# Optimization experiments

Measured on AMD Instinct MI355X. Metric: run time of the kernel, lower is better.

## Reference

```python
import jax, jax.numpy as jnp
import numpy as np

B = 2097152  # batch
H = 9        # hidden width
N_MID = 19   # fc2..fc20


def setup_inputs() -> dict:
    key = jax.random.key(0)
    ks = jax.random.split(key, 8)
    x = jax.random.normal(ks[0], (B, 2), dtype=jnp.float32)
    # PyTorch Linear init: U(-1/sqrt(fan_in), 1/sqrt(fan_in))
    def lin(k, out_f, in_f):
        kw, kb = jax.random.split(k)
        bound = 1.0 / np.sqrt(in_f)
        W = jax.random.uniform(kw, (out_f, in_f), jnp.float32, -bound, bound)
        b = jax.random.uniform(kb, (out_f,), jnp.float32, -bound, bound)
        return W, b
    W1, b1 = lin(ks[1], H, 2)
    # stacked middle layers fc2..fc20: [19, 9, 9] / [19, 9]
    kmids = jax.random.split(ks[2], N_MID)
    Wmid = jnp.stack([lin(k, H, H)[0] for k in kmids])
    bmid = jnp.stack([lin(jax.random.fold_in(k, 1), H, H)[1] for k in kmids])
    W21, b21 = lin(ks[3], 2, H)
    return {"x": x, "W1": W1, "b1": b1, "Wmid": Wmid, "bmid": bmid,
            "W21": W21, "b21": b21}


def reference(x, W1, b1, Wmid, bmid, W21, b21):
    h = jax.nn.elu(x @ W1.T + b1)  # [B, 9]
    def layer(h, wb):
        W, b = wb
        return jax.nn.elu(h @ W.T + b), None
    h, _ = jax.lax.scan(layer, h, (Wmid, bmid))
    logits = h @ W21.T + b21  # [B, 2]
    return jax.nn.log_softmax(logits, axis=1)
```

## Files before the change

kernel.cpp:

```cpp
#include <hip/hip_runtime.h>


typedef _Float16 half8 __attribute__((ext_vector_type(8)));
typedef float float4v __attribute__((ext_vector_type(4)));
typedef unsigned int uint4v __attribute__((ext_vector_type(4)));

constexpr int H   = 9;
constexpr int NL  = 21;
constexpr int TPW = 8;
constexpr int BLK = 256;

__global__ void build_frags(const float* __restrict__ W1, const float* __restrict__ b1,
                            const float* __restrict__ Wmid, const float* __restrict__ bmid,
                            const float* __restrict__ W21, const float* __restrict__ b21,
                            _Float16* __restrict__ ws) {
    const float L   = 1.4426950408889634f;
    const float LN2 = 0.6931471805599453f;
    int l    = blockIdx.x;
    int lane = threadIdx.x;
    int row  = lane & 15;
    int g    = lane >> 4;
    bool orow = ((row & 3) != 3) && (row < 12);
    int  o    = row - (row >> 2);
    for (int j = 0; j < 8; ++j) {
        int k = g * 8 + j;
        float v = 0.0f;
        if (l == 0) {
            if (orow && k < 2)        v = L * W1[o * 2 + k];
            else if (orow && k == 24) v = L * b1[o];
        } else if (l <= 19) {
            const float* W = Wmid + (l - 1) * 81;
            const float* b = bmid + (l - 1) * 9;
            if (orow) {
                if (j < 3 && g < 3) {
                    int r_in = g * 4 + j;
                    int i = r_in - (r_in >> 2);
                    v = W[o * 9 + i];
                } else if (j >= 4 && j < 7 && g < 3) {
                    int r_in = g * 4 + (j - 4);
                    int i = r_in - (r_in >> 2);
                    v = L * W[o * 9 + i];
                } else if (k == 24) {
                    float s = 0.0f;
                    for (int i = 0; i < H; ++i) s += W[o * 9 + i];
                    v = L * (b[o] - s);
                }
            }
        } else {
            if (row < 2) {
                if (j < 3 && g < 3) {
                    int r_in = g * 4 + j;
                    int i = r_in - (r_in >> 2);
                    v = LN2 * W21[row * 9 + i];
                } else if (j >= 4 && j < 7 && g < 3) {
                    int r_in = g * 4 + (j - 4);
                    int i = r_in - (r_in >> 2);
                    v = W21[row * 9 + i];
                } else if (k == 24) {
                    float s = 0.0f;
                    for (int i = 0; i < H; ++i) s += W21[row * 9 + i];
                    v = b21[row] - s;
                }
            }
        }
        ws[l * 512 + lane * 8 + j] = (_Float16)v;
    }
}

__device__ __forceinline__ half8 act_to_b(float4v d, unsigned bias_or) {
    float r0 = fmaxf(d[0], 0.f), r1 = fmaxf(d[1], 0.f), r2 = fmaxf(d[2], 0.f);
    float t0 = fminf(d[0], 0.f), t1 = fminf(d[1], 0.f), t2 = fminf(d[2], 0.f);
    float e0 = __builtin_amdgcn_exp2f(t0);
    float e1 = __builtin_amdgcn_exp2f(t1);
    float e2 = __builtin_amdgcn_exp2f(t2);
    uint4v u;
    u[0] = __builtin_bit_cast(unsigned, __builtin_amdgcn_cvt_pkrtz(r0, r1)) | bias_or;
    u[1] = __builtin_bit_cast(unsigned, __builtin_amdgcn_cvt_pkrtz(r2, 0.f));
    u[2] = __builtin_bit_cast(unsigned, __builtin_amdgcn_cvt_pkrtz(e0, e1));
    u[3] = __builtin_bit_cast(unsigned, __builtin_amdgcn_cvt_pkrtz(e2, 1.f));
    return __builtin_bit_cast(half8, u);
}

__device__ __forceinline__ half8 x_to_b(float2 xv, unsigned g0_sel, unsigned bias_or) {
    unsigned ux = __builtin_bit_cast(unsigned, __builtin_amdgcn_cvt_pkrtz(xv.x, xv.y));
    uint4v u;
    u[0] = (ux & g0_sel) | bias_or;
    u[1] = 0u; u[2] = 0u; u[3] = 0u;
    return __builtin_bit_cast(half8, u);
}

__device__ __forceinline__ float bperm(int byte_idx, float v) {
    return __builtin_bit_cast(float,
        __builtin_amdgcn_ds_bpermute(byte_idx, __builtin_bit_cast(int, v)));
}

__global__ __launch_bounds__(BLK, 2) void mlp_mfma(const float* __restrict__ x,
                                                   const _Float16* __restrict__ ws,
                                                   float* __restrict__ out) {
    const int lane = threadIdx.x & 63;
    const int wave = (blockIdx.x * BLK + threadIdx.x) >> 6;
    const int grp  = lane >> 4;
    const int col  = lane & 15;

    half8 A[NL];
    const half8* wsv = (const half8*)ws;
    #pragma unroll
    for (int l = 0; l < NL; ++l) A[l] = wsv[l * 64 + lane];

    const unsigned bias_or = (grp == 3) ? 0x00003C00u : 0u;
    const unsigned g0_sel  = (grp == 0) ? 0xFFFFFFFFu : 0u;
    const float4v ZV = {0.f, 0.f, 0.f, 0.f};
    const float NLOG2E = -1.4426950408889634f;
    const float LN2f   = 0.6931471805599453f;

    #pragma unroll 1
    for (int t = 0; t < TPW; t += 4) {
        const int tile0 = wave * TPW + t;

        half8 bf[4];
        #pragma unroll
        for (int k = 0; k < 4; ++k) {
            float2 xv = ((const float2*)x)[((tile0 + k) << 4) + col];
            bf[k] = x_to_b(xv, g0_sel, bias_or);
        }

        float4v dd[4];
        #pragma unroll
        for (int l = 0; l < NL; ++l) {
            #pragma unroll
            for (int k = 0; k < 4; ++k)
                dd[k] = __builtin_amdgcn_mfma_f32_16x16x32_f16(A[l], bf[k], ZV, 0, 0, 0);
            if (l < NL - 1) {
                #pragma unroll
                for (int k = 0; k < 4; ++k)
                    bf[k] = act_to_b(dd[k], bias_or);
            }
        }

        const int bidx = col << 2;
        float a0 = bperm(bidx, dd[0][0]), a1 = bperm(bidx, dd[0][1]);
        float b0 = bperm(bidx, dd[1][0]), b1 = bperm(bidx, dd[1][1]);
        float c0 = bperm(bidx, dd[2][0]), c1 = bperm(bidx, dd[2][1]);
        float d0 = bperm(bidx, dd[3][0]), d1 = bperm(bidx, dd[3][1]);
        float l0 = (grp == 0) ? a0 : (grp == 1) ? b0 : (grp == 2) ? c0 : d0;
        float l1 = (grp == 0) ? a1 : (grp == 1) ? b1 : (grp == 2) ? c1 : d1;

        float mx  = fmaxf(l0, l1);
        float ad  = fabsf(l0 - l1);
        float e   = __builtin_amdgcn_exp2f(NLOG2E * ad);
        float lg  = __builtin_amdgcn_logf(1.0f + e);
        float lse = fmaf(LN2f, lg, mx);
        ((float2*)out)[(tile0 << 4) + lane] = make_float2(l0 - lse, l1 - lse);
    }
}

extern "C" void kernel_launch(void* const* d_in, const int* in_sizes, int n_in,
                              void* d_out, int out_size, void* d_ws, size_t ws_size,
                              hipStream_t stream) {
    const float* x    = (const float*)d_in[0];
    const float* W1   = (const float*)d_in[1];
    const float* b1   = (const float*)d_in[2];
    const float* Wmid = (const float*)d_in[3];
    const float* bmid = (const float*)d_in[4];
    const float* W21  = (const float*)d_in[5];
    const float* b21  = (const float*)d_in[6];
    float* out = (float*)d_out;
    _Float16* ws = (_Float16*)d_ws;

    build_frags<<<NL, 64, 0, stream>>>(W1, b1, Wmid, bmid, W21, b21, ws);

    const int nrows = in_sizes[0] / 2;
    const int tiles = nrows / 16;
    const int waves = tiles / TPW;
    const int blocks = waves * 64 / BLK;
    mlp_mfma<<<blocks, BLK, 0, stream>>>(x, ws, out);
}
```

Before: 181.5 us.

## Use single-wave blocks, prefetch all inputs up front, pack ReLU in fp16

The block size drops to one wave (64 threads) and the launch bound changes to 4 blocks per CU. All eight x tiles are loaded at kernel start, before any compute, so global load latency overlaps the weight fragment loads. The two 4-tile groups are unrolled through a helper instead of a runtime loop. In the ELU activation, ReLU is applied as a packed fp16 max after conversion, replacing separate fp32 max ops. This raises register use for the prefetched inputs and changes the scheduling granularity.

Measured after the change: 176.9 us. 1.03x faster.

```diff
diff --git a/kernel.cpp b/kernel.cpp
--- a/kernel.cpp
+++ b/kernel.cpp
@@ -2,13 +2,14 @@
 
 
 typedef _Float16 half8 __attribute__((ext_vector_type(8)));
+typedef _Float16 h2 __attribute__((ext_vector_type(2)));
 typedef float float4v __attribute__((ext_vector_type(4)));
 typedef unsigned int uint4v __attribute__((ext_vector_type(4)));
 
 constexpr int H   = 9;
 constexpr int NL  = 21;
 constexpr int TPW = 8;
-constexpr int BLK = 256;
+constexpr int BLK = 64;
 
 __global__ void build_frags(const float* __restrict__ W1, const float* __restrict__ b1,
                             const float* __restrict__ Wmid, const float* __restrict__ bmid,
@@ -68,14 +69,20 @@
 }
 
 __device__ __forceinline__ half8 act_to_b(float4v d, unsigned bias_or) {
-    float r0 = fmaxf(d[0], 0.f), r1 = fmaxf(d[1], 0.f), r2 = fmaxf(d[2], 0.f);
-    float t0 = fminf(d[0], 0.f), t1 = fminf(d[1], 0.f), t2 = fminf(d[2], 0.f);
+    const h2 Z = {(_Float16)0.f, (_Float16)0.f};
+    h2 p01 = __builtin_bit_cast(h2, __builtin_amdgcn_cvt_pkrtz(d[0], d[1]));
+    h2 p2x = __builtin_bit_cast(h2, __builtin_amdgcn_cvt_pkrtz(d[2], 0.f));
+    h2 r01 = __builtin_elementwise_max(p01, Z);
+    h2 r2x = __builtin_elementwise_max(p2x, Z);
+    float t0 = fminf(d[0], 0.f);
+    float t1 = fminf(d[1], 0.f);
+    float t2 = fminf(d[2], 0.f);
     float e0 = __builtin_amdgcn_exp2f(t0);
     float e1 = __builtin_amdgcn_exp2f(t1);
     float e2 = __builtin_amdgcn_exp2f(t2);
     uint4v u;
-    u[0] = __builtin_bit_cast(unsigned, __builtin_amdgcn_cvt_pkrtz(r0, r1)) | bias_or;
-    u[1] = __builtin_bit_cast(unsigned, __builtin_amdgcn_cvt_pkrtz(r2, 0.f));
+    u[0] = __builtin_bit_cast(unsigned, r01) | bias_or;
+    u[1] = __builtin_bit_cast(unsigned, r2x);
     u[2] = __builtin_bit_cast(unsigned, __builtin_amdgcn_cvt_pkrtz(e0, e1));
     u[3] = __builtin_bit_cast(unsigned, __builtin_amdgcn_cvt_pkrtz(e2, 1.f));
     return __builtin_bit_cast(half8, u);
@@ -94,64 +101,72 @@
         __builtin_amdgcn_ds_bpermute(byte_idx, __builtin_bit_cast(int, v)));
 }
 
-__global__ __launch_bounds__(BLK, 2) void mlp_mfma(const float* __restrict__ x,
+__device__ __forceinline__ void run_group(const half8* __restrict__ A,
+                                          const float2* __restrict__ xv,
+                                          int gbase, int lane, int grp,
+                                          unsigned g0_sel, unsigned bias_or,
+                                          float* __restrict__ out) {
+    const float4v ZV = {0.f, 0.f, 0.f, 0.f};
+    const float NLOG2E = -1.4426950408889634f;
+    const float LN2f   = 0.6931471805599453f;
+    const int col = lane & 15;
+
+    half8 bf[4];
+    #pragma unroll
+    for (int k = 0; k < 4; ++k) bf[k] = x_to_b(xv[k], g0_sel, bias_or);
+
+    float4v dd[4];
+    #pragma unroll
+    for (int l = 0; l < NL; ++l) {
+        #pragma unroll
+        for (int k = 0; k < 4; ++k)
+            dd[k] = __builtin_amdgcn_mfma_f32_16x16x32_f16(A[l], bf[k], ZV, 0, 0, 0);
+        if (l < NL - 1) {
+            #pragma unroll
+            for (int k = 0; k < 4; ++k)
+                bf[k] = act_to_b(dd[k], bias_or);
+        }
+    }
+
+    const int bidx = col << 2;
+    float a0 = bperm(bidx, dd[0][0]), a1 = bperm(bidx, dd[0][1]);
+    float b0 = bperm(bidx, dd[1][0]), b1 = bperm(bidx, dd[1][1]);
+    float c0 = bperm(bidx, dd[2][0]), c1 = bperm(bidx, dd[2][1]);
+    float d0 = bperm(bidx, dd[3][0]), d1 = bperm(bidx, dd[3][1]);
+    float l0 = (grp == 0) ? a0 : (grp == 1) ? b0 : (grp == 2) ? c0 : d0;
+    float l1 = (grp == 0) ? a1 : (grp == 1) ? b1 : (grp == 2) ? c1 : d1;
+
+    float mx  = fmaxf(l0, l1);
+    float ad  = fabsf(l0 - l1);
+    float e   = __builtin_amdgcn_exp2f(NLOG2E * ad);
+    float lg  = __builtin_amdgcn_logf(1.0f + e);
+    float lse = fmaf(LN2f, lg, mx);
+    ((float2*)out)[(gbase << 4) + lane] = make_float2(l0 - lse, l1 - lse);
+}
+
+__global__ __launch_bounds__(BLK, 4) void mlp_mfma(const float* __restrict__ x,
                                                    const _Float16* __restrict__ ws,
                                                    float* __restrict__ out) {
-    const int lane = threadIdx.x & 63;
-    const int wave = (blockIdx.x * BLK + threadIdx.x) >> 6;
-    const int grp  = lane >> 4;
-    const int col  = lane & 15;
+    const int lane  = threadIdx.x;
+    const int grp   = lane >> 4;
+    const int col   = lane & 15;
+    const int tile0 = blockIdx.x * TPW;
 
     half8 A[NL];
     const half8* wsv = (const half8*)ws;
     #pragma unroll
     for (int l = 0; l < NL; ++l) A[l] = wsv[l * 64 + lane];
 
+    float2 xv[TPW];
+    #pragma unroll
+    for (int k = 0; k < TPW; ++k)
+        xv[k] = ((const float2*)x)[((tile0 + k) << 4) + col];
+
     const unsigned bias_or = (grp == 3) ? 0x00003C00u : 0u;
     const unsigned g0_sel  = (grp == 0) ? 0xFFFFFFFFu : 0u;
-    const float4v ZV = {0.f, 0.f, 0.f, 0.f};
-    const float NLOG2E = -1.4426950408889634f;
-    const float LN2f   = 0.6931471805599453f;
 
-    #pragma unroll 1
-    for (int t = 0; t < TPW; t += 4) {
-        const int tile0 = wave * TPW + t;
-
-        half8 bf[4];
-        #pragma unroll
-        for (int k = 0; k < 4; ++k) {
-            float2 xv = ((const float2*)x)[((tile0 + k) << 4) + col];
-            bf[k] = x_to_b(xv, g0_sel, bias_or);
-        }
-
-        float4v dd[4];
-        #pragma unroll
-        for (int l = 0; l < NL; ++l) {
-            #pragma unroll
-            for (int k = 0; k < 4; ++k)
-                dd[k] = __builtin_amdgcn_mfma_f32_16x16x32_f16(A[l], bf[k], ZV, 0, 0, 0);
-            if (l < NL - 1) {
-                #pragma unroll
-                for (int k = 0; k < 4; ++k)
-                    bf[k] = act_to_b(dd[k], bias_or);
-            }
-        }
-
-        const int bidx = col << 2;
-        float a0 = bperm(bidx, dd[0][0]), a1 = bperm(bidx, dd[0][1]);
-        float b0 = bperm(bidx, dd[1][0]), b1 = bperm(bidx, dd[1][1]);
-        float c0 = bperm(bidx, dd[2][0]), c1 = bperm(bidx, dd[2][1]);
-        float d0 = bperm(bidx, dd[3][0]), d1 = bperm(bidx, dd[3][1]);
-        float l0 = (grp == 0) ? a0 : (grp == 1) ? b0 : (grp == 2) ? c0 : d0;
-        float l1 = (grp == 0) ? a1 : (grp == 1) ? b1 : (grp == 2) ? c1 : d1;
-
-        float mx  = fmaxf(l0, l1);
-        float ad  = fabsf(l0 - l1);
-        float e   = __builtin_amdgcn_exp2f(NLOG2E * ad);
-        float lg  = __builtin_amdgcn_logf(1.0f + e);
-        float lse = fmaf(LN2f, lg, mx);
-        ((float2*)out)[(tile0 << 4) + lane] = make_float2(l0 - lse, l1 - lse);
-    }
+    run_group(A, xv,     tile0,     lane, grp, g0_sel, bias_or, out);
+    run_group(A, xv + 4, tile0 + 4, lane, grp, g0_sel, bias_or, out);
 }
 
 extern "C" void kernel_launch(void* const* d_in, const int* in_sizes, int n_in,
@@ -171,7 +186,6 @@
 
     const int nrows = in_sizes[0] / 2;
     const int tiles = nrows / 16;
-    const int waves = tiles / TPW;
-    const int blocks = waves * 64 / BLK;
+    const int blocks = tiles / TPW;
     mlp_mfma<<<blocks, BLK, 0, stream>>>(x, ws, out);
 }
```
